# Optimization experiments

Hardware: AMD Instinct MI355X
Metric: run time of the kernel (lower is better)

The kernel has to match this reference:

```python
import jax, jax.numpy as jnp
import numpy as np

C = 256          # hidden_size
H = 8            # num_heads
HD = C // H      # head dim = 32
W = 8            # window side; N = W*W = 64 tokens per window
N = W * W
NW = 64          # windows per image
B = 32           # images
B_ = B * NW      # 2048


def make_rel_index():
    # identical to the torch buffer construction (meshgrid 'ij')
    coords = np.stack(np.meshgrid(np.arange(W), np.arange(W), indexing='ij'))  # (2,W,W)
    flat = coords.reshape(2, -1)                       # (2, N)
    rel = flat[:, :, None] - flat[:, None, :]          # (2, N, N)
    rel = rel.transpose(1, 2, 0).astype(np.int64)      # (N, N, 2)
    rel[..., 0] += W - 1
    rel[..., 1] += W - 1
    rel[..., 0] *= 2 * W - 1
    return jnp.asarray(rel.sum(-1), jnp.int32)         # (N, N) in [0, 225)


def setup_inputs() -> dict:
    key = jax.random.key(0)
    ks = jax.random.split(key, 12)
    x = jax.random.normal(ks[0], (B_, N, C), jnp.float32)
    # Swin-style additive mask: 0 for allowed, -1e9 for masked pairs
    keep = jax.random.uniform(ks[1], (NW, N, N)) > 0.1
    mask = jnp.where(keep, 0.0, -1e9).astype(jnp.float32)
    std = 0.02
    wq = jax.random.normal(ks[2], (C, C), jnp.float32) * std
    bq = jnp.zeros((C,), jnp.float32)
    wk = jax.random.normal(ks[3], (C, C), jnp.float32) * std
    bk = jnp.zeros((C,), jnp.float32)
    wv = jax.random.normal(ks[4], (C, C), jnp.float32) * std
    bv = jnp.zeros((C,), jnp.float32)
    wp = jax.random.normal(ks[5], (C, C), jnp.float32) * std
    bp = jnp.zeros((C,), jnp.float32)
    bias_table = jax.random.normal(ks[6], ((2 * W - 1) ** 2, H), jnp.float32) * std
    rel_index = make_rel_index()
    return {"x": x, "mask": mask, "wq": wq, "bq": bq, "wk": wk, "bk": bk,
            "wv": wv, "bv": bv, "wp": wp, "bp": bp,
            "bias_table": bias_table, "rel_index": rel_index}


def reference(x, mask, wq, bq, wk, bk, wv, bv, wp, bp, bias_table, rel_index):
    B_, N, C = x.shape
    nW = mask.shape[0]
    H = bias_table.shape[1]
    HD = C // H
    scale = HD ** -0.5

    def heads(t):  # (B_, N, C) -> (B_, H, N, HD)
        return t.reshape(B_, N, H, HD).transpose(0, 2, 1, 3)

    q = heads(x @ wq + bq) * scale
    k = heads(x @ wk + bk)
    v = heads(x @ wv + bv)

    attn = jnp.einsum('bhnd,bhmd->bhnm', q, k)            # (B_, H, N, N)
    bias = bias_table[rel_index]                          # (N, N, H)
    attn = attn + bias.transpose(2, 0, 1)[None]           # + (1, H, N, N)
    # add per-window shift mask, broadcast over batch and heads
    attn = attn.reshape(B_ // nW, nW, H, N, N) + mask[None, :, None]
    attn = jax.nn.softmax(attn.reshape(B_, H, N, N), axis=-1)

    out = jnp.einsum('bhnm,bhmd->bhnd', attn, v)          # (B_, H, N, HD)
    out = out.transpose(0, 2, 1, 3).reshape(B_, N, C)
    return out @ wp + bp
```

## Files before the change

### kernel.cpp

```cpp
#include <hip/hip_runtime.h>
#include <hip/hip_bf16.h>

typedef __bf16 bf16;
typedef __bf16 bf16x4 __attribute__((ext_vector_type(4)));
typedef __bf16 bf16x8 __attribute__((ext_vector_type(8)));
typedef float  f32x4  __attribute__((ext_vector_type(4)));
typedef short  s16x4  __attribute__((ext_vector_type(4)));

#define DEVI __device__ __forceinline__

static constexpr float kScale = 0.17677669529663687f;

DEVI f32x4 mfma32(bf16x8 a, bf16x8 b, f32x4 c) {
  return __builtin_amdgcn_mfma_f32_16x16x32_bf16(a, b, c, 0, 0, 0);
}
DEVI f32x4 mfma16(bf16x4 a, bf16x4 b, f32x4 c) {
#if __has_builtin(__builtin_amdgcn_mfma_f32_16x16x16bf16_1k)
  return __builtin_amdgcn_mfma_f32_16x16x16bf16_1k(
      __builtin_bit_cast(s16x4, a), __builtin_bit_cast(s16x4, b), c, 0, 0, 0);
#else
  f32x4 d;
  asm volatile("v_mfma_f32_16x16x16_bf16 %0, %1, %2, %3"
               : "=v"(d)
               : "v"(a), "v"(b), "v"(c));
  return d;
#endif
}
DEVI bf16x4 pk4(f32x4 v) {
  bf16x4 p;
  p[0] = (bf16)v[0]; p[1] = (bf16)v[1]; p[2] = (bf16)v[2]; p[3] = (bf16)v[3];
  return p;
}

__global__ __launch_bounds__(256) void prep_kernel(
    const float* __restrict__ wq, const float* __restrict__ bq,
    const float* __restrict__ wk, const float* __restrict__ bk,
    const float* __restrict__ wv, const float* __restrict__ bv,
    const float* __restrict__ wp,
    const float* __restrict__ bias_table, const int* __restrict__ rel_index,
    const float* __restrict__ mask,
    char* __restrict__ wsall, float* __restrict__ bqkv, bf16* __restrict__ biasM) {
  int idx = blockIdx.x * 256 + threadIdx.x;
  if (idx < 196608) {
    int m = idx >> 16, n = idx & 255, k = (idx >> 8) & 255;
    const float* w = (m == 0) ? wq : (m == 1 ? wk : wv);
    float v = w[k * 256 + n];
    if (m == 0) v *= kScale;
    *(bf16*)(wsall + (size_t)(m * 4 + (k >> 6)) * 32768 + n * 128 +
             (((k & 63) * 2) ^ ((n & 7) << 4))) = (bf16)v;
  } else if (idx < 262144) {
    int rem = idx - 196608;
    int n = rem & 255, k = (rem >> 8) & 255;
    *(bf16*)(wsall + (size_t)(12 + (k >> 6)) * 32768 + n * 128 +
             (((k & 63) * 2) ^ ((n & 7) << 4))) = (bf16)wp[k * 256 + n];
  } else if (idx < 262912) {
    int rem = idx - 262144;
    int m = rem >> 8, n = rem & 255;
    const float* b = (m == 0) ? bq : (m == 1 ? bk : bv);
    float v = b[n];
    if (m == 0) v *= kScale;
    bqkv[rem] = v;
  } else if (idx < 2360064) {
    int rem = idx - 262912;
    int w = rem >> 15, h = (rem >> 12) & 7, ij = rem & 4095;
    biasM[rem] = (bf16)(bias_table[rel_index[ij] * 8 + h] + mask[w * 4096 + ij]);
  }
}

__global__ __launch_bounds__(512, 1) void swin_kernel(
    const float* __restrict__ x, const char* __restrict__ wsall,
    const float* __restrict__ bqkv, const float* __restrict__ bp,
    const bf16* __restrict__ biasM, float* __restrict__ out) {
  __shared__ __align__(16) char xs_ob[65536];
  __shared__ __align__(16) char wbuf[65536];

  int tid = threadIdx.x;
  int w = tid >> 6, lane = tid & 63;
  int g = lane >> 4, c = lane & 15;
  int hw = w >> 2, s = w & 3;
  int win = blockIdx.x * 2 + hw;
  char* xs = xs_ob + hw * 32768;
  const f32x4 fz = {0.f, 0.f, 0.f, 0.f};

  {
    int hw2 = tid >> 8, t256 = tid & 255;
    const char* xw = (const char*)x + ((size_t)blockIdx.x * 2 + hw2) * 65536;
    char* xd = xs_ob + hw2 * 32768;
#pragma unroll
    for (int i = 0; i < 8; ++i) {
      int gb = i * 8192 + t256 * 32;
      float4 f0 = *(const float4*)(xw + gb);
      float4 f1 = *(const float4*)(xw + gb + 16);
      bf16x8 v;
      v[0] = (bf16)f0.x; v[1] = (bf16)f0.y; v[2] = (bf16)f0.z; v[3] = (bf16)f0.w;
      v[4] = (bf16)f1.x; v[5] = (bf16)f1.y; v[6] = (bf16)f1.z; v[7] = (bf16)f1.w;
      int t = gb >> 10, ir = (gb & 1023) >> 1;
      *(bf16x8*)(xd + ((t * 512 + ir) ^ ((t & 7) << 4))) = v;
    }
  }
  bf16x8 gr[4];
#pragma unroll
  for (int j = 0; j < 4; ++j)
    gr[j] = *(const bf16x8*)(wsall + (size_t)j * 8192 + (size_t)tid * 16);
#pragma unroll
  for (int j = 0; j < 4; ++j)
    *(bf16x8*)(wbuf + j * 8192 + tid * 16) = gr[j];
#pragma unroll
  for (int j = 0; j < 4; ++j)
    gr[j] = *(const bf16x8*)(wsall + 32768 + (size_t)j * 8192 + (size_t)tid * 16);
  __syncthreads();

  bf16x4 qp[4][4], kp[4][4], vp[4][4];
  f32x4 acc[4][4];

  for (int i = 0; i < 12; ++i) {
    int m = i >> 2, kc = i & 3;
    char* cur = wbuf + (i & 1) * 32768;
    char* nxt = wbuf + ((i + 1) & 1) * 32768;

    if (kc == 0) {
      if (m < 2) {
#pragma unroll
        for (int nt = 0; nt < 4; ++nt) {
          f32x4 b4 = *(const f32x4*)(bqkv + m * 256 + s * 64 + nt * 16 + g * 4);
#pragma unroll
          for (int tt = 0; tt < 4; ++tt) acc[tt][nt] = b4;
        }
      } else {
#pragma unroll
        for (int nt = 0; nt < 4; ++nt) {
          float bv_ = bqkv[512 + s * 64 + nt * 16 + c];
          f32x4 b4 = {bv_, bv_, bv_, bv_};
#pragma unroll
          for (int tt = 0; tt < 4; ++tt) acc[tt][nt] = b4;
        }
      }
    }
#pragma unroll
    for (int kq2 = 0; kq2 < 2; ++kq2) {
      bf16x8 xf[4], wf[4];
#pragma unroll
      for (int tt = 0; tt < 4; ++tt)
        xf[tt] = *(const bf16x8*)(
            xs + (((tt * 16 + c) * 512 + kc * 128 + kq2 * 64 + g * 16) ^ ((c & 7) << 4)));
#pragma unroll
      for (int nt = 0; nt < 4; ++nt)
        wf[nt] = *(const bf16x8*)(
            cur + (s * 64 + nt * 16 + c) * 128 + ((kq2 * 64 + g * 16) ^ ((c & 7) << 4)));
      if (m < 2) {
#pragma unroll
        for (int tt = 0; tt < 4; ++tt)
#pragma unroll
          for (int nt = 0; nt < 4; ++nt)
            acc[tt][nt] = mfma32(wf[nt], xf[tt], acc[tt][nt]);
      } else {
#pragma unroll
        for (int tt = 0; tt < 4; ++tt)
#pragma unroll
          for (int nt = 0; nt < 4; ++nt)
            acc[tt][nt] = mfma32(xf[tt], wf[nt], acc[tt][nt]);
      }
    }
    if (kc == 3) {
#pragma unroll
      for (int tt = 0; tt < 4; ++tt)
#pragma unroll
        for (int nt = 0; nt < 4; ++nt) {
          if (m == 0)      qp[tt][nt] = pk4(acc[tt][nt]);
          else if (m == 1) kp[tt][nt] = pk4(acc[tt][nt]);
          else             vp[tt][nt] = pk4(acc[tt][nt]);
        }
    }
#pragma unroll
    for (int j = 0; j < 4; ++j)
      *(bf16x8*)(nxt + j * 8192 + tid * 16) = gr[j];
    if (i + 2 <= 15) {
#pragma unroll
      for (int j = 0; j < 4; ++j)
        gr[j] = *(const bf16x8*)(wsall + (size_t)(i + 2) * 32768 +
                                 (size_t)j * 8192 + (size_t)tid * 16);
    }
    __syncthreads();
  }

#pragma unroll
  for (int hh = 0; hh < 2; ++hh) {
    int h = s * 2 + hh;
    const bf16* bm = biasM + ((size_t)(win & 63) * 8 + h) * 4096;
#pragma unroll
    for (int mi = 0; mi < 4; ++mi) {
      f32x4 sv[4];
#pragma unroll
      for (int mj = 0; mj < 4; ++mj) {
        bf16x4 b4 = *(const bf16x4*)(bm + (mi * 16 + c) * 64 + mj * 16 + g * 4);
        sv[mj] = (f32x4){(float)b4[0], (float)b4[1], (float)b4[2], (float)b4[3]};
      }
#pragma unroll
      for (int dd = 0; dd < 2; ++dd)
#pragma unroll
        for (int mj = 0; mj < 4; ++mj)
          sv[mj] = mfma16(kp[mj][hh * 2 + dd], qp[mi][hh * 2 + dd], sv[mj]);
      float mx;
      {
        f32x4 m4 = sv[0];
#pragma unroll
        for (int mj = 1; mj < 4; ++mj) {
          m4[0] = fmaxf(m4[0], sv[mj][0]); m4[1] = fmaxf(m4[1], sv[mj][1]);
          m4[2] = fmaxf(m4[2], sv[mj][2]); m4[3] = fmaxf(m4[3], sv[mj][3]);
        }
        mx = fmaxf(fmaxf(m4[0], m4[1]), fmaxf(m4[2], m4[3]));
        mx = fmaxf(mx, __shfl_xor(mx, 16));
        mx = fmaxf(mx, __shfl_xor(mx, 32));
      }
      float sum;
      {
        f32x4 s4 = fz;
#pragma unroll
        for (int mj = 0; mj < 4; ++mj) {
#pragma unroll
          for (int r = 0; r < 4; ++r) sv[mj][r] = __expf(sv[mj][r] - mx);
          s4 += sv[mj];
        }
        sum = (s4[0] + s4[1]) + (s4[2] + s4[3]);
        sum += __shfl_xor(sum, 16);
        sum += __shfl_xor(sum, 32);
      }
      float rs = 1.0f / sum;
      bf16x4 pf[4];
#pragma unroll
      for (int mj = 0; mj < 4; ++mj) pf[mj] = pk4(sv[mj]);
#pragma unroll
      for (int dt = 0; dt < 2; ++dt) {
        f32x4 o = fz;
#pragma unroll
        for (int mj = 0; mj < 4; ++mj)
          o = mfma16(vp[mj][hh * 2 + dt], pf[mj], o);
        bf16x4 ov;
        ov[0] = (bf16)(o[0] * rs); ov[1] = (bf16)(o[1] * rs);
        ov[2] = (bf16)(o[2] * rs); ov[3] = (bf16)(o[3] * rs);
        *(bf16x4*)(xs + (((mi * 16 + c) * 512 + (h * 32 + dt * 16 + g * 4) * 2) ^
                         ((c & 7) << 4))) = ov;
      }
    }
  }
  __syncthreads();

  f32x4 acc2[4][4];
#pragma unroll
  for (int nt = 0; nt < 4; ++nt) {
    f32x4 b4 = *(const f32x4*)(bp + s * 64 + nt * 16 + g * 4);
#pragma unroll
    for (int tt = 0; tt < 4; ++tt) acc2[tt][nt] = b4;
  }
  for (int i = 12; i < 16; ++i) {
    int kc = i - 12;
    char* cur = wbuf + (i & 1) * 32768;
    char* nxt = wbuf + ((i + 1) & 1) * 32768;
#pragma unroll
    for (int kq2 = 0; kq2 < 2; ++kq2) {
      bf16x8 of[4], wf[4];
#pragma unroll
      for (int tt = 0; tt < 4; ++tt)
        of[tt] = *(const bf16x8*)(
            xs + (((tt * 16 + c) * 512 + kc * 128 + kq2 * 64 + g * 16) ^ ((c & 7) << 4)));
#pragma unroll
      for (int nt = 0; nt < 4; ++nt)
        wf[nt] = *(const bf16x8*)(
            cur + (s * 64 + nt * 16 + c) * 128 + ((kq2 * 64 + g * 16) ^ ((c & 7) << 4)));
#pragma unroll
      for (int tt = 0; tt < 4; ++tt)
#pragma unroll
        for (int nt = 0; nt < 4; ++nt)
          acc2[tt][nt] = mfma32(wf[nt], of[tt], acc2[tt][nt]);
    }
    if (i < 15) {
#pragma unroll
      for (int j = 0; j < 4; ++j)
        *(bf16x8*)(nxt + j * 8192 + tid * 16) = gr[j];
      if (i + 2 <= 15) {
#pragma unroll
        for (int j = 0; j < 4; ++j)
          gr[j] = *(const bf16x8*)(wsall + (size_t)(i + 2) * 32768 +
                                   (size_t)j * 8192 + (size_t)tid * 16);
      }
      __syncthreads();
    }
  }
#pragma unroll
  for (int tt = 0; tt < 4; ++tt)
#pragma unroll
    for (int nt = 0; nt < 4; ++nt)
      *(f32x4*)(out + ((size_t)win * 64 + tt * 16 + c) * 256 + s * 64 + nt * 16 + g * 4) =
          acc2[tt][nt];
}

extern "C" void kernel_launch(void* const* d_in, const int* in_sizes, int n_in,
                              void* d_out, int out_size, void* d_ws, size_t ws_size,
                              hipStream_t stream) {
  const float* x          = (const float*)d_in[0];
  const float* mask       = (const float*)d_in[1];
  const float* wq         = (const float*)d_in[2];
  const float* bq         = (const float*)d_in[3];
  const float* wk         = (const float*)d_in[4];
  const float* bk         = (const float*)d_in[5];
  const float* wv         = (const float*)d_in[6];
  const float* bv         = (const float*)d_in[7];
  const float* wp         = (const float*)d_in[8];
  const float* bp         = (const float*)d_in[9];
  const float* bias_table = (const float*)d_in[10];
  const int*   rel_index  = (const int*)d_in[11];

  char* ws = (char*)d_ws;
  size_t o = 0;
  char* wsall = ws + o; o += (size_t)16 * 32768;
  float* bqkv = (float*)(ws + o); o += (size_t)768 * 4;
  bf16* biasM = (bf16*)(ws + o); o += (size_t)64 * 8 * 64 * 64 * 2;
  if (ws_size < o) return;

  prep_kernel<<<9219, 256, 0, stream>>>(wq, bq, wk, bk, wv, bv, wp,
                                        bias_table, rel_index, mask,
                                        wsall, bqkv, biasM);
  swin_kernel<<<1024, 512, 0, stream>>>(x, wsall, bqkv, bp, biasM, (float*)d_out);
}
```

Baseline: 155.7 us.

## Process one window per 256-thread block with smaller single-buffered weight chunks

Result: slower. 236.0 us (+51.6%).

```diff
diff --git a/kernel.cpp b/kernel.cpp
--- a/kernel.cpp
+++ b/kernel.cpp
@@ -46,13 +46,15 @@
     const float* w = (m == 0) ? wq : (m == 1 ? wk : wv);
     float v = w[k * 256 + n];
     if (m == 0) v *= kScale;
-    *(bf16*)(wsall + (size_t)(m * 4 + (k >> 6)) * 32768 + n * 128 +
-             (((k & 63) * 2) ^ ((n & 7) << 4))) = (bf16)v;
+    int slot = (n ^ (n >> 2)) & 3;
+    *(bf16*)(wsall + (size_t)(m * 8 + (k >> 5)) * 16384 + n * 64 +
+             (((k & 31) * 2) ^ (slot << 4))) = (bf16)v;
   } else if (idx < 262144) {
     int rem = idx - 196608;
     int n = rem & 255, k = (rem >> 8) & 255;
-    *(bf16*)(wsall + (size_t)(12 + (k >> 6)) * 32768 + n * 128 +
-             (((k & 63) * 2) ^ ((n & 7) << 4))) = (bf16)wp[k * 256 + n];
+    int slot = (n ^ (n >> 2)) & 3;
+    *(bf16*)(wsall + (size_t)(24 + (k >> 5)) * 16384 + n * 64 +
+             (((k & 31) * 2) ^ (slot << 4))) = (bf16)wp[k * 256 + n];
   } else if (idx < 262912) {
     int rem = idx - 262144;
     int m = rem >> 8, n = rem & 255;
@@ -67,57 +69,52 @@
   }
 }
 
-__global__ __launch_bounds__(512, 1) void swin_kernel(
+__global__ __launch_bounds__(256, 1) void swin_kernel(
     const float* __restrict__ x, const char* __restrict__ wsall,
     const float* __restrict__ bqkv, const float* __restrict__ bp,
     const bf16* __restrict__ biasM, float* __restrict__ out) {
-  __shared__ __align__(16) char xs_ob[65536];
-  __shared__ __align__(16) char wbuf[65536];
+  __shared__ __align__(16) char xs_ob[32768];
+  __shared__ __align__(16) char wbuf[16384];
 
   int tid = threadIdx.x;
-  int w = tid >> 6, lane = tid & 63;
+  int s = tid >> 6, lane = tid & 63;
   int g = lane >> 4, c = lane & 15;
-  int hw = w >> 2, s = w & 3;
-  int win = blockIdx.x * 2 + hw;
-  char* xs = xs_ob + hw * 32768;
+  int win = blockIdx.x;
   const f32x4 fz = {0.f, 0.f, 0.f, 0.f};
+  int slot = (c ^ (c >> 2)) & 3;
 
   {
-    int hw2 = tid >> 8, t256 = tid & 255;
-    const char* xw = (const char*)x + ((size_t)blockIdx.x * 2 + hw2) * 65536;
-    char* xd = xs_ob + hw2 * 32768;
+    const char* xw = (const char*)(x + (size_t)win * 16384);
 #pragma unroll
     for (int i = 0; i < 8; ++i) {
-      int gb = i * 8192 + t256 * 32;
+      int gb = i * 8192 + tid * 32;
       float4 f0 = *(const float4*)(xw + gb);
       float4 f1 = *(const float4*)(xw + gb + 16);
       bf16x8 v;
       v[0] = (bf16)f0.x; v[1] = (bf16)f0.y; v[2] = (bf16)f0.z; v[3] = (bf16)f0.w;
       v[4] = (bf16)f1.x; v[5] = (bf16)f1.y; v[6] = (bf16)f1.z; v[7] = (bf16)f1.w;
       int t = gb >> 10, ir = (gb & 1023) >> 1;
-      *(bf16x8*)(xd + ((t * 512 + ir) ^ ((t & 7) << 4))) = v;
+      *(bf16x8*)(xs_ob + ((t * 512 + ir) ^ ((t & 7) << 4))) = v;
     }
   }
   bf16x8 gr[4];
 #pragma unroll
   for (int j = 0; j < 4; ++j)
-    gr[j] = *(const bf16x8*)(wsall + (size_t)j * 8192 + (size_t)tid * 16);
+    gr[j] = *(const bf16x8*)(wsall + (size_t)j * 4096 + (size_t)tid * 16);
 #pragma unroll
   for (int j = 0; j < 4; ++j)
-    *(bf16x8*)(wbuf + j * 8192 + tid * 16) = gr[j];
-#pragma unroll
-  for (int j = 0; j < 4; ++j)
-    gr[j] = *(const bf16x8*)(wsall + 32768 + (size_t)j * 8192 + (size_t)tid * 16);
+    *(bf16x8*)(wbuf + j * 4096 + tid * 16) = gr[j];
   __syncthreads();
 
   bf16x4 qp[4][4], kp[4][4], vp[4][4];
   f32x4 acc[4][4];
 
-  for (int i = 0; i < 12; ++i) {
-    int m = i >> 2, kc = i & 3;
-    char* cur = wbuf + (i & 1) * 32768;
-    char* nxt = wbuf + ((i + 1) & 1) * 32768;
-
+  for (int ci = 0; ci < 24; ++ci) {
+    int m = ci >> 3, kc = ci & 7;
+#pragma unroll
+    for (int j = 0; j < 4; ++j)
+      gr[j] = *(const bf16x8*)(wsall + (size_t)(ci + 1) * 16384 +
+                               (size_t)j * 4096 + (size_t)tid * 16);
     if (kc == 0) {
       if (m < 2) {
 #pragma unroll
@@ -136,17 +133,16 @@
         }
       }
     }
-#pragma unroll
-    for (int kq2 = 0; kq2 < 2; ++kq2) {
+    {
       bf16x8 xf[4], wf[4];
 #pragma unroll
       for (int tt = 0; tt < 4; ++tt)
         xf[tt] = *(const bf16x8*)(
-            xs + (((tt * 16 + c) * 512 + kc * 128 + kq2 * 64 + g * 16) ^ ((c & 7) << 4)));
+            xs_ob + (((tt * 16 + c) * 512 + kc * 64 + g * 16) ^ ((c & 7) << 4)));
 #pragma unroll
       for (int nt = 0; nt < 4; ++nt)
         wf[nt] = *(const bf16x8*)(
-            cur + (s * 64 + nt * 16 + c) * 128 + ((kq2 * 64 + g * 16) ^ ((c & 7) << 4)));
+            wbuf + (s * 64 + nt * 16 + c) * 64 + ((g * 16) ^ (slot << 4)));
       if (m < 2) {
 #pragma unroll
         for (int tt = 0; tt < 4; ++tt)
@@ -161,7 +157,7 @@
             acc[tt][nt] = mfma32(xf[tt], wf[nt], acc[tt][nt]);
       }
     }
-    if (kc == 3) {
+    if (kc == 7) {
 #pragma unroll
       for (int tt = 0; tt < 4; ++tt)
 #pragma unroll
@@ -171,17 +167,16 @@
           else             vp[tt][nt] = pk4(acc[tt][nt]);
         }
     }
+    __syncthreads();
 #pragma unroll
     for (int j = 0; j < 4; ++j)
-      *(bf16x8*)(nxt + j * 8192 + tid * 16) = gr[j];
-    if (i + 2 <= 15) {
-#pragma unroll
-      for (int j = 0; j < 4; ++j)
-        gr[j] = *(const bf16x8*)(wsall + (size_t)(i + 2) * 32768 +
-                                 (size_t)j * 8192 + (size_t)tid * 16);
-    }
+      *(bf16x8*)(wbuf + j * 4096 + tid * 16) = gr[j];
     __syncthreads();
   }
+#pragma unroll
+  for (int j = 0; j < 4; ++j)
+    gr[j] = *(const bf16x8*)(wsall + (size_t)25 * 16384 +
+                             (size_t)j * 4096 + (size_t)tid * 16);
 
 #pragma unroll
   for (int hh = 0; hh < 2; ++hh) {
@@ -238,8 +233,8 @@
         bf16x4 ov;
         ov[0] = (bf16)(o[0] * rs); ov[1] = (bf16)(o[1] * rs);
         ov[2] = (bf16)(o[2] * rs); ov[3] = (bf16)(o[3] * rs);
-        *(bf16x4*)(xs + (((mi * 16 + c) * 512 + (h * 32 + dt * 16 + g * 4) * 2) ^
-                         ((c & 7) << 4))) = ov;
+        *(bf16x4*)(xs_ob + (((mi * 16 + c) * 512 + (h * 32 + dt * 16 + g * 4) * 2) ^
+                            ((c & 7) << 4))) = ov;
       }
     }
   }
@@ -252,37 +247,35 @@
 #pragma unroll
     for (int tt = 0; tt < 4; ++tt) acc2[tt][nt] = b4;
   }
-  for (int i = 12; i < 16; ++i) {
-    int kc = i - 12;
-    char* cur = wbuf + (i & 1) * 32768;
-    char* nxt = wbuf + ((i + 1) & 1) * 32768;
-#pragma unroll
-    for (int kq2 = 0; kq2 < 2; ++kq2) {
+  for (int ci = 24; ci < 32; ++ci) {
+    int kc = ci - 24;
+    if (ci > 24 && ci < 31) {
+#pragma unroll
+      for (int j = 0; j < 4; ++j)
+        gr[j] = *(const bf16x8*)(wsall + (size_t)(ci + 1) * 16384 +
+                                 (size_t)j * 4096 + (size_t)tid * 16);
+    }
+    {
       bf16x8 of[4], wf[4];
 #pragma unroll
       for (int tt = 0; tt < 4; ++tt)
         of[tt] = *(const bf16x8*)(
-            xs + (((tt * 16 + c) * 512 + kc * 128 + kq2 * 64 + g * 16) ^ ((c & 7) << 4)));
+            xs_ob + (((tt * 16 + c) * 512 + kc * 64 + g * 16) ^ ((c & 7) << 4)));
 #pragma unroll
       for (int nt = 0; nt < 4; ++nt)
         wf[nt] = *(const bf16x8*)(
-            cur + (s * 64 + nt * 16 + c) * 128 + ((kq2 * 64 + g * 16) ^ ((c & 7) << 4)));
+            wbuf + (s * 64 + nt * 16 + c) * 64 + ((g * 16) ^ (slot << 4)));
 #pragma unroll
       for (int tt = 0; tt < 4; ++tt)
 #pragma unroll
         for (int nt = 0; nt < 4; ++nt)
           acc2[tt][nt] = mfma32(wf[nt], of[tt], acc2[tt][nt]);
     }
-    if (i < 15) {
+    if (ci < 31) {
+      __syncthreads();
 #pragma unroll
       for (int j = 0; j < 4; ++j)
-        *(bf16x8*)(nxt + j * 8192 + tid * 16) = gr[j];
-      if (i + 2 <= 15) {
-#pragma unroll
-        for (int j = 0; j < 4; ++j)
-          gr[j] = *(const bf16x8*)(wsall + (size_t)(i + 2) * 32768 +
-                                   (size_t)j * 8192 + (size_t)tid * 16);
-      }
+        *(bf16x8*)(wbuf + j * 4096 + tid * 16) = gr[j];
       __syncthreads();
     }
   }
@@ -312,7 +305,7 @@
 
   char* ws = (char*)d_ws;
   size_t o = 0;
-  char* wsall = ws + o; o += (size_t)16 * 32768;
+  char* wsall = ws + o; o += (size_t)32 * 16384;
   float* bqkv = (float*)(ws + o); o += (size_t)768 * 4;
   bf16* biasM = (bf16*)(ws + o); o += (size_t)64 * 8 * 64 * 64 * 2;
   if (ws_size < o) return;
@@ -320,5 +313,5 @@
   prep_kernel<<<9219, 256, 0, stream>>>(wq, bq, wk, bk, wv, bv, wp,
                                         bias_table, rel_index, mask,
                                         wsall, bqkv, biasM);
-  swin_kernel<<<1024, 512, 0, stream>>>(x, wsall, bqkv, bp, biasM, (float*)d_out);
-}
+  swin_kernel<<<2048, 256, 0, stream>>>(x, wsall, bqkv, bp, biasM, (float*)d_out);
+}
```

## Double-buffer weight prefetch registers to issue global loads a full step earlier

Applied to the files above, without the earlier changes.

Result: slower. 161.4 us (+3.7%).

```diff
diff --git a/kernel.cpp b/kernel.cpp
--- a/kernel.cpp
+++ b/kernel.cpp
@@ -82,6 +82,14 @@
   char* xs = xs_ob + hw * 32768;
   const f32x4 fz = {0.f, 0.f, 0.f, 0.f};
 
+  bf16x8 grA[4], grB[4];
+#pragma unroll
+  for (int j = 0; j < 4; ++j)
+    grA[j] = *(const bf16x8*)(wsall + (size_t)j * 8192 + (size_t)tid * 16);
+#pragma unroll
+  for (int j = 0; j < 4; ++j)
+    grB[j] = *(const bf16x8*)(wsall + 32768 + (size_t)j * 8192 + (size_t)tid * 16);
+
   {
     int hw2 = tid >> 8, t256 = tid & 255;
     const char* xw = (const char*)x + ((size_t)blockIdx.x * 2 + hw2) * 65536;
@@ -98,90 +106,79 @@
       *(bf16x8*)(xd + ((t * 512 + ir) ^ ((t & 7) << 4))) = v;
     }
   }
-  bf16x8 gr[4];
 #pragma unroll
   for (int j = 0; j < 4; ++j)
-    gr[j] = *(const bf16x8*)(wsall + (size_t)j * 8192 + (size_t)tid * 16);
-#pragma unroll
-  for (int j = 0; j < 4; ++j)
-    *(bf16x8*)(wbuf + j * 8192 + tid * 16) = gr[j];
-#pragma unroll
-  for (int j = 0; j < 4; ++j)
-    gr[j] = *(const bf16x8*)(wsall + 32768 + (size_t)j * 8192 + (size_t)tid * 16);
+    *(bf16x8*)(wbuf + j * 8192 + tid * 16) = grA[j];
   __syncthreads();
 
   bf16x4 qp[4][4], kp[4][4], vp[4][4];
   f32x4 acc[4][4];
 
-  for (int i = 0; i < 12; ++i) {
-    int m = i >> 2, kc = i & 3;
-    char* cur = wbuf + (i & 1) * 32768;
-    char* nxt = wbuf + ((i + 1) & 1) * 32768;
-
-    if (kc == 0) {
-      if (m < 2) {
-#pragma unroll
-        for (int nt = 0; nt < 4; ++nt) {
-          f32x4 b4 = *(const f32x4*)(bqkv + m * 256 + s * 64 + nt * 16 + g * 4);
-#pragma unroll
-          for (int tt = 0; tt < 4; ++tt) acc[tt][nt] = b4;
-        }
-      } else {
-#pragma unroll
-        for (int nt = 0; nt < 4; ++nt) {
-          float bv_ = bqkv[512 + s * 64 + nt * 16 + c];
-          f32x4 b4 = {bv_, bv_, bv_, bv_};
-#pragma unroll
-          for (int tt = 0; tt < 4; ++tt) acc[tt][nt] = b4;
-        }
-      }
-    }
-#pragma unroll
-    for (int kq2 = 0; kq2 < 2; ++kq2) {
-      bf16x8 xf[4], wf[4];
-#pragma unroll
-      for (int tt = 0; tt < 4; ++tt)
-        xf[tt] = *(const bf16x8*)(
-            xs + (((tt * 16 + c) * 512 + kc * 128 + kq2 * 64 + g * 16) ^ ((c & 7) << 4)));
-#pragma unroll
-      for (int nt = 0; nt < 4; ++nt)
-        wf[nt] = *(const bf16x8*)(
-            cur + (s * 64 + nt * 16 + c) * 128 + ((kq2 * 64 + g * 16) ^ ((c & 7) << 4)));
-      if (m < 2) {
-#pragma unroll
-        for (int tt = 0; tt < 4; ++tt)
-#pragma unroll
-          for (int nt = 0; nt < 4; ++nt)
-            acc[tt][nt] = mfma32(wf[nt], xf[tt], acc[tt][nt]);
-      } else {
-#pragma unroll
-        for (int tt = 0; tt < 4; ++tt)
-#pragma unroll
-          for (int nt = 0; nt < 4; ++nt)
-            acc[tt][nt] = mfma32(xf[tt], wf[nt], acc[tt][nt]);
-      }
-    }
-    if (kc == 3) {
-#pragma unroll
-      for (int tt = 0; tt < 4; ++tt)
-#pragma unroll
-        for (int nt = 0; nt < 4; ++nt) {
-          if (m == 0)      qp[tt][nt] = pk4(acc[tt][nt]);
-          else if (m == 1) kp[tt][nt] = pk4(acc[tt][nt]);
-          else             vp[tt][nt] = pk4(acc[tt][nt]);
-        }
-    }
-#pragma unroll
-    for (int j = 0; j < 4; ++j)
-      *(bf16x8*)(nxt + j * 8192 + tid * 16) = gr[j];
-    if (i + 2 <= 15) {
-#pragma unroll
-      for (int j = 0; j < 4; ++j)
-        gr[j] = *(const bf16x8*)(wsall + (size_t)(i + 2) * 32768 +
-                                 (size_t)j * 8192 + (size_t)tid * 16);
-    }
-    __syncthreads();
-  }
+#define QKV_STEP(CI, GRI, GRW)                                                  \
+  {                                                                             \
+    int ci = (CI);                                                              \
+    if (ci + 2 <= 15) {                                                         \
+      _Pragma("unroll") for (int j = 0; j < 4; ++j)                             \
+        GRI[j] = *(const bf16x8*)(wsall + (size_t)(ci + 2) * 32768 +            \
+                                  (size_t)j * 8192 + (size_t)tid * 16);         \
+    }                                                                           \
+    int m = ci >> 2, kc = ci & 3;                                               \
+    char* cur = wbuf + (ci & 1) * 32768;                                        \
+    char* nxt = wbuf + ((ci + 1) & 1) * 32768;                                  \
+    if (kc == 0) {                                                              \
+      if (m < 2) {                                                              \
+        _Pragma("unroll") for (int nt = 0; nt < 4; ++nt) {                      \
+          f32x4 b4 = *(const f32x4*)(bqkv + m * 256 + s * 64 + nt * 16 + g * 4);\
+          _Pragma("unroll") for (int tt = 0; tt < 4; ++tt) acc[tt][nt] = b4;    \
+        }                                                                       \
+      } else {                                                                  \
+        _Pragma("unroll") for (int nt = 0; nt < 4; ++nt) {                      \
+          float bv_ = bqkv[512 + s * 64 + nt * 16 + c];                         \
+          f32x4 b4 = {bv_, bv_, bv_, bv_};                                      \
+          _Pragma("unroll") for (int tt = 0; tt < 4; ++tt) acc[tt][nt] = b4;    \
+        }                                                                       \
+      }                                                                         \
+    }                                                                           \
+    _Pragma("unroll") for (int kq2 = 0; kq2 < 2; ++kq2) {                       \
+      bf16x8 xf[4], wf[4];                                                      \
+      _Pragma("unroll") for (int tt = 0; tt < 4; ++tt)                          \
+        xf[tt] = *(const bf16x8*)(xs + (((tt * 16 + c) * 512 + kc * 128 +       \
+                                         kq2 * 64 + g * 16) ^ ((c & 7) << 4))); \
+      _Pragma("unroll") for (int nt = 0; nt < 4; ++nt)                          \
+        wf[nt] = *(const bf16x8*)(cur + (s * 64 + nt * 16 + c) * 128 +          \
+                                  ((kq2 * 64 + g * 16) ^ ((c & 7) << 4)));      \
+      if (m < 2) {                                                              \
+        _Pragma("unroll") for (int tt = 0; tt < 4; ++tt)                        \
+          _Pragma("unroll") for (int nt = 0; nt < 4; ++nt)                      \
+            acc[tt][nt] = mfma32(wf[nt], xf[tt], acc[tt][nt]);                  \
+      } else {                                                                  \
+        _Pragma("unroll") for (int tt = 0; tt < 4; ++tt)                        \
+          _Pragma("unroll") for (int nt = 0; nt < 4; ++nt)                      \
+            acc[tt][nt] = mfma32(xf[tt], wf[nt], acc[tt][nt]);                  \
+      }                                                                         \
+    }                                                                           \
+    if (kc == 3) {                                                              \
+      _Pragma("unroll") for (int tt = 0; tt < 4; ++tt)                          \
+        _Pragma("unroll") for (int nt = 0; nt < 4; ++nt) {                      \
+          if (m == 0)      qp[tt][nt] = pk4(acc[tt][nt]);                       \
+          else if (m == 1) kp[tt][nt] = pk4(acc[tt][nt]);                       \
+          else             vp[tt][nt] = pk4(acc[tt][nt]);                       \
+        }                                                                       \
+    }                                                                           \
+    _Pragma("unroll") for (int j = 0; j < 4; ++j)                               \
+      *(bf16x8*)(nxt + j * 8192 + tid * 16) = GRW[j];                           \
+    __syncthreads();                                                            \
+  }
+
+  for (int cp = 0; cp < 6; ++cp) {
+    QKV_STEP(cp * 2,     grA, grB);
+    QKV_STEP(cp * 2 + 1, grB, grA);
+  }
+#undef QKV_STEP
+#pragma unroll
+  for (int j = 0; j < 4; ++j)
+    grA[j] = *(const bf16x8*)(wsall + (size_t)14 * 32768 +
+                              (size_t)j * 8192 + (size_t)tid * 16);
 
 #pragma unroll
   for (int hh = 0; hh < 2; ++hh) {
@@ -252,40 +249,41 @@
 #pragma unroll
     for (int tt = 0; tt < 4; ++tt) acc2[tt][nt] = b4;
   }
-  for (int i = 12; i < 16; ++i) {
-    int kc = i - 12;
-    char* cur = wbuf + (i & 1) * 32768;
-    char* nxt = wbuf + ((i + 1) & 1) * 32768;
-#pragma unroll
-    for (int kq2 = 0; kq2 < 2; ++kq2) {
-      bf16x8 of[4], wf[4];
-#pragma unroll
-      for (int tt = 0; tt < 4; ++tt)
-        of[tt] = *(const bf16x8*)(
-            xs + (((tt * 16 + c) * 512 + kc * 128 + kq2 * 64 + g * 16) ^ ((c & 7) << 4)));
-#pragma unroll
-      for (int nt = 0; nt < 4; ++nt)
-        wf[nt] = *(const bf16x8*)(
-            cur + (s * 64 + nt * 16 + c) * 128 + ((kq2 * 64 + g * 16) ^ ((c & 7) << 4)));
-#pragma unroll
-      for (int tt = 0; tt < 4; ++tt)
-#pragma unroll
-        for (int nt = 0; nt < 4; ++nt)
-          acc2[tt][nt] = mfma32(wf[nt], of[tt], acc2[tt][nt]);
-    }
-    if (i < 15) {
-#pragma unroll
-      for (int j = 0; j < 4; ++j)
-        *(bf16x8*)(nxt + j * 8192 + tid * 16) = gr[j];
-      if (i + 2 <= 15) {
-#pragma unroll
-        for (int j = 0; j < 4; ++j)
-          gr[j] = *(const bf16x8*)(wsall + (size_t)(i + 2) * 32768 +
-                                   (size_t)j * 8192 + (size_t)tid * 16);
-      }
-      __syncthreads();
-    }
-  }
+#define PROJ_STEP(CI, GRW, ISSUE15)                                             \
+  {                                                                             \
+    int ci = (CI);                                                              \
+    int kc = ci - 12;                                                           \
+    char* cur = wbuf + (ci & 1) * 32768;                                        \
+    char* nxt = wbuf + ((ci + 1) & 1) * 32768;                                  \
+    if (ISSUE15) {                                                              \
+      _Pragma("unroll") for (int j = 0; j < 4; ++j)                             \
+        grB[j] = *(const bf16x8*)(wsall + (size_t)15 * 32768 +                  \
+                                  (size_t)j * 8192 + (size_t)tid * 16);         \
+    }                                                                           \
+    _Pragma("unroll") for (int kq2 = 0; kq2 < 2; ++kq2) {                       \
+      bf16x8 of[4], wf[4];                                                      \
+      _Pragma("unroll") for (int tt = 0; tt < 4; ++tt)                          \
+        of[tt] = *(const bf16x8*)(xs + (((tt * 16 + c) * 512 + kc * 128 +       \
+                                         kq2 * 64 + g * 16) ^ ((c & 7) << 4))); \
+      _Pragma("unroll") for (int nt = 0; nt < 4; ++nt)                          \
+        wf[nt] = *(const bf16x8*)(cur + (s * 64 + nt * 16 + c) * 128 +          \
+                                  ((kq2 * 64 + g * 16) ^ ((c & 7) << 4)));      \
+      _Pragma("unroll") for (int tt = 0; tt < 4; ++tt)                          \
+        _Pragma("unroll") for (int nt = 0; nt < 4; ++nt)                        \
+          acc2[tt][nt] = mfma32(wf[nt], of[tt], acc2[tt][nt]);                  \
+    }                                                                           \
+    if (ci < 15) {                                                              \
+      _Pragma("unroll") for (int j = 0; j < 4; ++j)                             \
+        *(bf16x8*)(nxt + j * 8192 + tid * 16) = GRW[j];                         \
+      __syncthreads();                                                          \
+    }                                                                           \
+  }
+  PROJ_STEP(12, grB, 0);
+  PROJ_STEP(13, grA, 1);
+  PROJ_STEP(14, grB, 0);
+  PROJ_STEP(15, grA, 0);
+#undef PROJ_STEP
+
 #pragma unroll
   for (int tt = 0; tt < 4; ++tt)
 #pragma unroll
```
